# Optimization experiments

Hardware: AMD Instinct MI355X
Metric: run time of the kernel (lower is better)

The kernel has to match this reference:

```python
import jax, jax.numpy as jnp
import numpy as np
import math

B, T = 16, 512
P = 256          # num_memory_positions
E = 128          # embedding_dim
NB = 4           # num_beings
K = 4            # attention_radius
TEMP = 8.0       # attention_temperature
PHI = 1.618033988749895


def setup_inputs() -> dict:
    key = jax.random.key(0)
    ks = jax.random.split(key, 8)
    x = jax.random.normal(ks[0], (B, T, 8), jnp.float32)
    W_in = jax.random.normal(ks[1], (8, E), jnp.float32) * 0.1
    b_in = jnp.zeros((E,), jnp.float32)
    W_out = jax.random.normal(ks[2], (E, 8), jnp.float32) * 0.1
    b_out = jnp.zeros((8,), jnp.float32)
    W_p = jax.random.normal(ks[3], (E, E), jnp.float32) * (1.0 / np.sqrt(E))
    b_p = jnp.zeros((E,), jnp.float32)
    ptr_dest = jax.random.uniform(ks[4], (NB, P), jnp.float32) * P
    jump_W = jax.random.normal(ks[5], (NB, E), jnp.float32) * 0.1
    jump_b = jnp.zeros((NB,), jnp.float32)
    ctx_strength = jnp.full((NB,), 0.2, jnp.float32)
    pe = np.zeros((NB, E), np.float32)
    for i in range(NB):
        ph = i * PHI
        v = []
        for h in range(1, 9):
            v += [math.sin(h * ph), math.cos(h * ph)]
        pe[i, :16] = v  # phase_embedding padded with zeros to E (E >= 16)
    phase_bias = jnp.asarray(pe)
    seg = P / NB
    pointer_init = jax.random.uniform(ks[6], (NB, B), jnp.float32) * seg + jnp.arange(NB, dtype=jnp.float32)[:, None] * seg
    return dict(x=x, W_in=W_in, b_in=b_in, W_out=W_out, b_out=b_out,
                W_p=W_p, b_p=b_p, ptr_dest=ptr_dest, jump_W=jump_W,
                jump_b=jump_b, ctx_strength=ctx_strength,
                phase_bias=phase_bias, pointer_init=pointer_init)


def _forward(x, W_in, b_in, W_out, b_out, W_p, b_p, ptr_dest, jump_W,
             jump_b, ctx_strength, phase_bias, pointer_init):
    offsets = jnp.arange(-K, K + 1)          # [W]
    b_ix = jnp.arange(B)                     # [B]
    half = P / 2.0
    ring0 = jnp.zeros((B, P, E), x.dtype)
    hid0 = jnp.zeros((NB, B, E), x.dtype)

    def step(carry, x_t):
        ring, ptrs, hids = carry
        inp = x_t @ W_in + b_in              # [B,E]
        outs, new_ptrs, new_hids = [], [], []
        for i in range(NB):                  # beings sequential (share ring)
            ptr, hid = ptrs[i], hids[i]
            base = jnp.clip(jnp.floor(ptr).astype(jnp.int32), 0, P - 1)
            idx = (base[:, None] + offsets[None, :]) % P            # [B,W]
            delta = jnp.mod(idx.astype(x_t.dtype) - ptr[:, None] + half, P) - half
            w = jax.nn.softmax(-(delta ** 2) / TEMP, axis=1)         # [B,W]
            nbhd = ring[b_ix[:, None], idx]                          # [B,W,E]
            ctx = jnp.sum(w[..., None] * nbhd, axis=1)               # [B,E]
            comb = inp + jax.nn.sigmoid(ctx_strength[i]) * ctx + 0.1 * phase_bias[i]
            s = jnp.tanh(comb + hid)
            s = jnp.tanh(s @ W_p + b_p)      # depth-1 = 1 processing layer
            ring = ring.at[b_ix[:, None], idx].add(w[..., None] * s[:, None, :])
            cur = jnp.clip(ptr.astype(jnp.int32), 0, P - 1)
            jump_target = ptr_dest[i][cur]                           # [B]
            probs = jax.nn.sigmoid(s @ jump_W[i] + jump_b[i])        # [B]
            hard = (probs > 0.5).astype(s.dtype)
            should_jump = hard - jax.lax.stop_gradient(probs) + probs
            walk = (ptr + 1.0) % P
            new_ptrs.append(jnp.where(should_jump > 0.5, jump_target, walk))
            new_hids.append(s)
            outs.append(s @ W_out + b_out)                           # [B,8]
        out_t = jnp.mean(jnp.stack(outs), axis=0)                    # [B,8] (training-mode mean)
        return (ring, jnp.stack(new_ptrs), jnp.stack(new_hids)), out_t

    _, ys = jax.lax.scan(step, (ring0, pointer_init, hid0), jnp.swapaxes(x, 0, 1))
    return jnp.swapaxes(ys, 0, 1)            # [B,T,8]


def reference(x, W_in, b_in, W_out, b_out, W_p, b_p, ptr_dest, jump_W,
              jump_b, ctx_strength, phase_bias, pointer_init):
    return _forward(x, W_in, b_in, W_out, b_out, W_p, b_p, ptr_dest,
                    jump_W, jump_b, ctx_strength, phase_bias, pointer_init)
```

## Files before the change

### kernel.cpp

```cpp
#include <hip/hip_runtime.h>
#include <cmath>

namespace {
constexpr int B_ = 16, T_ = 512, P_ = 256, E_ = 128, NB_ = 4, K_ = 4;

__device__ __forceinline__ float rcpf(float x) { return __builtin_amdgcn_rcpf(x); }
__device__ __forceinline__ float fast_tanh(float x) {
    float a = fabsf(x);
    float t = __expf(-2.0f * a);
    float r = 1.0f - 2.0f * t * rcpf(1.0f + t);
    return copysignf(r, x);
}
__device__ __forceinline__ float redkq(float v) {
    v += __shfl_xor(v, 16);
    v += __shfl_xor(v, 32);
    return v;
}
__device__ __forceinline__ float sel4(int kq, float a, float b, float c, float d) {
    const float t0 = (kq & 1) ? b : a;
    const float t1 = (kq & 1) ? d : c;
    return (kq & 2) ? t1 : t0;
}
}

__global__ __launch_bounds__(256, 1)
void swarm_ring_kernel(const float* __restrict__ x,
                       const float* __restrict__ W_in,
                       const float* __restrict__ b_in,
                       const float* __restrict__ W_out,
                       const float* __restrict__ b_out,
                       const float* __restrict__ W_p,
                       const float* __restrict__ b_p,
                       const float* __restrict__ ptr_dest,
                       const float* __restrict__ jump_W,
                       const float* __restrict__ jump_b,
                       const float* __restrict__ ctx_strength,
                       const float* __restrict__ phase_bias,
                       const float* __restrict__ pointer_init,
                       float* __restrict__ out)
{
    __shared__ alignas(16) float  ring[P_ * E_];
    __shared__ alignas(16) float4 s4[E_];
    __shared__ alignas(16) float  sbuf[2 * E_];
    __shared__ alignas(16) float  red[16];
    __shared__ alignas(16) float  hist[16][132];
    __shared__ alignas(16) float  wout_s[8][132];

    const int tid = threadIdx.x;
    const int b   = blockIdx.x;
    const int w   = tid >> 6;
    const int l   = tid & 63;
    const int sub = l & 15;
    const int kq  = l >> 4;
    const int e0  = ((w << 4) | sub) << 1;

    for (int k4 = tid; k4 < P_ * E_ / 4; k4 += 256)
        ((float4*)ring)[k4] = make_float4(0.f, 0.f, 0.f, 0.f);
    for (int idx = tid; idx < 8 * E_; idx += 256) {
        const int m = idx >> 7, ee = idx & 127;
        wout_s[m][ee] = W_out[ee * 8 + m] * 0.25f;
    }

    float2 wp2[32];
    #pragma unroll
    for (int kk = 0; kk < 32; ++kk)
        wp2[kk] = *(const float2*)(W_p + (kq * 32 + kk) * E_ + e0);

    const float2 bin2 = *(const float2*)(b_in + e0);
    const float2 bp2  = *(const float2*)(b_p + e0);
    const float  bout_m = b_out[tid & 7];

    float2 pb2[NB_], jw2[NB_], hid2[NB_];
    float  sigc[NB_], jb_r[NB_], ptrv[NB_];
    #pragma unroll
    for (int i = 0; i < NB_; ++i) {
        const float2 pb = *(const float2*)(phase_bias + i * E_ + e0);
        pb2[i] = make_float2(0.1f * pb.x, 0.1f * pb.y);
        jw2[i] = *(const float2*)(jump_W + i * E_ + e0);
        sigc[i] = 1.0f / (1.0f + __expf(-ctx_strength[i]));
        jb_r[i] = jump_b[i];
        hid2[i] = make_float2(0.f, 0.f);
        ptrv[i] = pointer_init[i * B_ + b];
    }

    const float* xb = x + (size_t)b * T_ * 8;
    float xt[8];
    {
        float4 a0 = ((const float4*)xb)[0], a1 = ((const float4*)xb)[1];
        xt[0]=a0.x; xt[1]=a0.y; xt[2]=a0.z; xt[3]=a0.w;
        xt[4]=a1.x; xt[5]=a1.y; xt[6]=a1.z; xt[7]=a1.w;
    }

    const float Cw1 = 0.8824969f, Cw2 = 0.60653066f, Cw3 = 0.32465247f, Cw4 = 0.13533528f;
    const float Dw1 = 0.7788008f, Dw2 = 0.36787944f, Dw3 = 0.105399225f, Dw4 = 0.018315639f;

    __syncthreads();

    for (int t = 0; t < T_; ++t) {
        int   baseA[NB_];
        float fA[NB_], psinv[NB_], jt[NB_], wgt[NB_][9];
        #pragma unroll
        for (int i = 0; i < NB_; ++i) {
            const float p = ptrv[i];
            const int base = (int)p;
            baseA[i] = base;
            jt[i] = ptr_dest[i * P_ + base];
            const float f = p - (float)base;
            fA[i] = f;
            const float r  = __expf(0.25f * f);
            const float r2 = r * r, r3 = r2 * r, r4 = r2 * r2;
            const float ri = rcpf(r), ri2 = ri * ri, ri3 = ri2 * ri, ri4 = ri2 * ri2;
            const float p0 = Cw4*ri4, p1 = Cw3*ri3, p2 = Cw2*ri2, p3 = Cw1*ri, p4 = 1.0f,
                        p5 = Cw1*r,  p6 = Cw2*r2,  p7 = Cw3*r3,  p8 = Cw4*r4;
            const float sum = ((p0+p1)+(p2+p3)) + ((p4+p5)+(p6+p7)) + p8;
            const float inv = rcpf(sum);
            psinv[i] = inv;
            wgt[i][0]=p0*inv; wgt[i][1]=p1*inv; wgt[i][2]=p2*inv; wgt[i][3]=p3*inv;
            wgt[i][4]=p4*inv; wgt[i][5]=p5*inv; wgt[i][6]=p6*inv; wgt[i][7]=p7*inv;
            wgt[i][8]=p8*inv;
        }

        int ddm[NB_][NB_];
        bool overlap = false;
        #pragma unroll
        for (int j = 1; j < NB_; ++j)
            #pragma unroll
            for (int i = 0; i < j; ++i) {
                const int dd = ((baseA[j] - baseA[i] + 128) & 255) - 128;
                ddm[j][i] = dd;
                overlap = overlap || (dd >= -8 && dd <= 8);
            }

        float  ws0[NB_], ws1[NB_];
        float2 ctxp2[NB_];
        #pragma unroll
        for (int i = 0; i < NB_; ++i) {
            ws0[i] = sel4(kq, wgt[i][0], wgt[i][1], wgt[i][2], wgt[i][3]);
            ws1[i] = sel4(kq, wgt[i][4], wgt[i][5], wgt[i][6], wgt[i][7]);
            const int r0 = (baseA[i] + kq - K_) & (P_ - 1);
            const int r1 = (baseA[i] + kq + 4 - K_) & (P_ - 1);
            const float2 g0 = *(const float2*)(ring + r0 * E_ + e0);
            const float2 g1 = *(const float2*)(ring + r1 * E_ + e0);
            float cx = fmaf(ws1[i], g1.x, ws0[i] * g0.x);
            float cy = fmaf(ws1[i], g1.y, ws0[i] * g0.y);
            if (kq == 0) {
                const int r2 = (baseA[i] + 8 - K_) & (P_ - 1);
                const float2 g2 = *(const float2*)(ring + r2 * E_ + e0);
                cx = fmaf(wgt[i][8], g2.x, cx);
                cy = fmaf(wgt[i][8], g2.y, cy);
            }
            ctxp2[i] = make_float2(redkq(cx), redkq(cy));
        }

        float2 inp2 = bin2;
        #pragma unroll
        for (int k = 0; k < 8; ++k) {
            const float2 wk = *(const float2*)(W_in + k * E_ + e0);
            inp2.x = fmaf(xt[k], wk.x, inp2.x);
            inp2.y = fmaf(xt[k], wk.y, inp2.y);
        }

        float xtn[8];
        if (t + 1 < T_) {
            float4 a0 = ((const float4*)(xb + (t + 1) * 8))[0];
            float4 a1 = ((const float4*)(xb + (t + 1) * 8))[1];
            xtn[0]=a0.x; xtn[1]=a0.y; xtn[2]=a0.z; xtn[3]=a0.w;
            xtn[4]=a1.x; xtn[5]=a1.y; xtn[6]=a1.z; xtn[7]=a1.w;
        } else {
            #pragma unroll
            for (int k = 0; k < 8; ++k) xtn[k] = 0.f;
        }

        float2 sv2[NB_];

        if (!overlap) {
            float2 s1v[NB_];
            #pragma unroll
            for (int j = 0; j < NB_; ++j) {
                s1v[j].x = fast_tanh(fmaf(sigc[j], ctxp2[j].x, inp2.x + pb2[j].x + hid2[j].x));
                s1v[j].y = fast_tanh(fmaf(sigc[j], ctxp2[j].y, inp2.y + pb2[j].y + hid2[j].y));
            }
            if (kq == 0) {
                s4[e0]     = make_float4(s1v[0].x, s1v[1].x, s1v[2].x, s1v[3].x);
                s4[e0 + 1] = make_float4(s1v[0].y, s1v[1].y, s1v[2].y, s1v[3].y);
            }
            __syncthreads();

            float2 ab0 = make_float2(0.f, 0.f), ab1 = ab0, ab2 = ab0, ab3 = ab0;
            const float4* sp = s4 + kq * 32;
            #pragma unroll
            for (int kk = 0; kk < 32; ++kk) {
                const float4 sq = sp[kk];
                const float2 w2 = wp2[kk];
                ab0.x = fmaf(sq.x, w2.x, ab0.x); ab0.y = fmaf(sq.x, w2.y, ab0.y);
                ab1.x = fmaf(sq.y, w2.x, ab1.x); ab1.y = fmaf(sq.y, w2.y, ab1.y);
                ab2.x = fmaf(sq.z, w2.x, ab2.x); ab2.y = fmaf(sq.z, w2.y, ab2.y);
                ab3.x = fmaf(sq.w, w2.x, ab3.x); ab3.y = fmaf(sq.w, w2.y, ab3.y);
            }
            sv2[0] = make_float2(fast_tanh(redkq(ab0.x) + bp2.x), fast_tanh(redkq(ab0.y) + bp2.y));
            sv2[1] = make_float2(fast_tanh(redkq(ab1.x) + bp2.x), fast_tanh(redkq(ab1.y) + bp2.y));
            sv2[2] = make_float2(fast_tanh(redkq(ab2.x) + bp2.x), fast_tanh(redkq(ab2.y) + bp2.y));
            sv2[3] = make_float2(fast_tanh(redkq(ab3.x) + bp2.x), fast_tanh(redkq(ab3.y) + bp2.y));
            #pragma unroll
            for (int j = 0; j < NB_; ++j) hid2[j] = sv2[j];

            #pragma unroll
            for (int j = 0; j < NB_; ++j) {
                const float2 s = sv2[j];
                const int r0 = (baseA[j] + kq - K_) & (P_ - 1);
                float2* q0 = (float2*)(ring + r0 * E_ + e0);
                float2 v0 = *q0;
                v0.x = fmaf(ws0[j], s.x, v0.x); v0.y = fmaf(ws0[j], s.y, v0.y);
                *q0 = v0;
                const int r1 = (baseA[j] + kq + 4 - K_) & (P_ - 1);
                float2* q1 = (float2*)(ring + r1 * E_ + e0);
                float2 v1 = *q1;
                v1.x = fmaf(ws1[j], s.x, v1.x); v1.y = fmaf(ws1[j], s.y, v1.y);
                *q1 = v1;
                if (kq == 0) {
                    const int r2 = (baseA[j] + 8 - K_) & (P_ - 1);
                    float2* q2 = (float2*)(ring + r2 * E_ + e0);
                    float2 v2 = *q2;
                    v2.x = fmaf(wgt[j][8], s.x, v2.x); v2.y = fmaf(wgt[j][8], s.y, v2.y);
                    *q2 = v2;
                }
            }
        } else {
            float coefm[NB_][NB_];
            #pragma unroll
            for (int j = 1; j < NB_; ++j) {
                #pragma unroll
                for (int i = 0; i < j; ++i) {
                    const int dd = ddm[j][i];
                    float c = 0.f;
                    if (dd >= -8 && dd <= 8) {
                        const float A = (float)dd - fA[i];
                        const float s  = __expf(-0.25f * (A - fA[j]));
                        const float G  = __expf(0.125f * (fA[i] * fA[i] - A * A));
                        const float s2p = s * s, s3p = s2p * s, s4p = s2p * s2p;
                        const float si = rcpf(s), si2 = si * si, si3 = si2 * si, si4 = si2 * si2;
                        float acc = 0.f;
                        acc += (dd >= 0)              ? Dw4 * si4 : 0.f;
                        acc += (dd >= -1 && dd <= 7)  ? Dw3 * si3 : 0.f;
                        acc += (dd >= -2 && dd <= 6)  ? Dw2 * si2 : 0.f;
                        acc += (dd >= -3 && dd <= 5)  ? Dw1 * si  : 0.f;
                        acc += (dd >= -4 && dd <= 4)  ? 1.0f      : 0.f;
                        acc += (dd >= -5 && dd <= 3)  ? Dw1 * s   : 0.f;
                        acc += (dd >= -6 && dd <= 2)  ? Dw2 * s2p : 0.f;
                        acc += (dd >= -7 && dd <= 1)  ? Dw3 * s3p : 0.f;
                        acc += (dd <= 0)              ? Dw4 * s4p : 0.f;
                        c = psinv[i] * psinv[j] * G * acc;
                    }
                    coefm[j][i] = c;
                }
            }

            #pragma unroll
            for (int j = 0; j < NB_; ++j) {
                float2 ctx = ctxp2[j];
                #pragma unroll
                for (int i = 0; i < j; ++i) {
                    ctx.x = fmaf(coefm[j][i], sv2[i].x, ctx.x);
                    ctx.y = fmaf(coefm[j][i], sv2[i].y, ctx.y);
                }
                float2 s1;
                s1.x = fast_tanh(fmaf(sigc[j], ctx.x, inp2.x + pb2[j].x + hid2[j].x));
                s1.y = fast_tanh(fmaf(sigc[j], ctx.y, inp2.y + pb2[j].y + hid2[j].y));
                if (kq == 0) *(float2*)(sbuf + (j & 1) * E_ + e0) = s1;
                __syncthreads();

                const float4* sp = (const float4*)(sbuf + (j & 1) * E_) + kq * 8;
                float ax = 0.f, ay = 0.f;
                #pragma unroll
                for (int kk = 0; kk < 8; ++kk) {
                    const float4 sq = sp[kk];
                    const float2 wa = wp2[4 * kk + 0], wb = wp2[4 * kk + 1];
                    const float2 wc = wp2[4 * kk + 2], wd = wp2[4 * kk + 3];
                    ax = fmaf(sq.x, wa.x, ax); ay = fmaf(sq.x, wa.y, ay);
                    ax = fmaf(sq.y, wb.x, ax); ay = fmaf(sq.y, wb.y, ay);
                    ax = fmaf(sq.z, wc.x, ax); ay = fmaf(sq.z, wc.y, ay);
                    ax = fmaf(sq.w, wd.x, ax); ay = fmaf(sq.w, wd.y, ay);
                }
                float2 s2;
                s2.x = fast_tanh(redkq(ax) + bp2.x);
                s2.y = fast_tanh(redkq(ay) + bp2.y);
                sv2[j] = s2; hid2[j] = s2;

                const int r0 = (baseA[j] + kq - K_) & (P_ - 1);
                float2* q0 = (float2*)(ring + r0 * E_ + e0);
                float2 v0 = *q0;
                v0.x = fmaf(ws0[j], s2.x, v0.x); v0.y = fmaf(ws0[j], s2.y, v0.y);
                *q0 = v0;
                const int r1 = (baseA[j] + kq + 4 - K_) & (P_ - 1);
                float2* q1 = (float2*)(ring + r1 * E_ + e0);
                float2 v1 = *q1;
                v1.x = fmaf(ws1[j], s2.x, v1.x); v1.y = fmaf(ws1[j], s2.y, v1.y);
                *q1 = v1;
                if (kq == 0) {
                    const int r2 = (baseA[j] + 8 - K_) & (P_ - 1);
                    float2* q2 = (float2*)(ring + r2 * E_ + e0);
                    float2 v2 = *q2;
                    v2.x = fmaf(wgt[j][8], s2.x, v2.x); v2.y = fmaf(wgt[j][8], s2.y, v2.y);
                    *q2 = v2;
                }
            }
        }

        {
            float vj0 = fmaf(sv2[0].y, jw2[0].y, sv2[0].x * jw2[0].x);
            float vj1 = fmaf(sv2[1].y, jw2[1].y, sv2[1].x * jw2[1].x);
            float vj2 = fmaf(sv2[2].y, jw2[2].y, sv2[2].x * jw2[2].x);
            float vj3 = fmaf(sv2[3].y, jw2[3].y, sv2[3].x * jw2[3].x);
            #pragma unroll
            for (int off = 1; off < 16; off <<= 1) {
                vj0 += __shfl_xor(vj0, off);
                vj1 += __shfl_xor(vj1, off);
                vj2 += __shfl_xor(vj2, off);
                vj3 += __shfl_xor(vj3, off);
            }
            if (l == 0)
                ((float4*)red)[w] = make_float4(vj0, vj1, vj2, vj3);
        }

        {
            float2 ssum2;
            ssum2.x = (sv2[0].x + sv2[1].x) + (sv2[2].x + sv2[3].x);
            ssum2.y = (sv2[0].y + sv2[1].y) + (sv2[2].y + sv2[3].y);
            if (kq == 0) *(float2*)(&hist[t & 15][e0]) = ssum2;
        }

        __syncthreads();

        {
            const float4 r0 = ((const float4*)red)[0];
            const float4 r1 = ((const float4*)red)[1];
            const float4 r2 = ((const float4*)red)[2];
            const float4 r3 = ((const float4*)red)[3];
            const float zz[4] = {
                ((r0.x + r1.x) + (r2.x + r3.x)) + jb_r[0],
                ((r0.y + r1.y) + (r2.y + r3.y)) + jb_r[1],
                ((r0.z + r1.z) + (r2.z + r3.z)) + jb_r[2],
                ((r0.w + r1.w) + (r2.w + r3.w)) + jb_r[3]};
            #pragma unroll
            for (int i = 0; i < NB_; ++i) {
                float np;
                if (zz[i] > 0.0f) np = jt[i];
                else { np = ptrv[i] + 1.0f; if (np >= 256.0f) np -= 256.0f; }
                ptrv[i] = np;
            }
        }

        if ((t & 7) == 7 && tid < 64) {
            const int tt = tid >> 3;
            const int m  = tid & 7;
            const float* hrow = hist[(t - 7 + tt) & 15];
            const float* wrow = wout_s[m];
            float acc = 0.f;
            #pragma unroll
            for (int q = 0; q < 32; ++q) {
                const float4 h4 = ((const float4*)hrow)[q];
                const float4 w4 = ((const float4*)wrow)[q];
                acc += ((h4.x * w4.x + h4.y * w4.y) + (h4.z * w4.z + h4.w * w4.w));
            }
            out[((size_t)b * T_ + (t - 7 + tt)) * 8 + m] = acc + bout_m;
        }

        #pragma unroll
        for (int k = 0; k < 8; ++k) xt[k] = xtn[k];
    }
}

extern "C" void kernel_launch(void* const* d_in, const int* in_sizes, int n_in,
                              void* d_out, int out_size, void* d_ws, size_t ws_size,
                              hipStream_t stream) {
    (void)in_sizes; (void)n_in; (void)out_size; (void)d_ws; (void)ws_size;
    swarm_ring_kernel<<<dim3(B_), dim3(256), 0, stream>>>(
        (const float*)d_in[0],  (const float*)d_in[1],  (const float*)d_in[2],
        (const float*)d_in[3],  (const float*)d_in[4],  (const float*)d_in[5],
        (const float*)d_in[6],  (const float*)d_in[7],  (const float*)d_in[8],
        (const float*)d_in[9],  (const float*)d_in[10], (const float*)d_in[11],
        (const float*)d_in[12], (float*)d_out);
}
```

Before: 2.056 ms.

## Double threads per block so each thread handles one embedding column

Raises the block from 256 to 512 threads so each lane owns a single embedding element instead of a pair. This halves the per-thread serial work in the latency-bound recurrent step. The shared-memory state buffer gets padding (stride 33) and the jump-logit reduction grows from 4 to 8 wave partials. The cost is twice as many waves meeting at each barrier and more shuffle and reduction traffic per step.

```diff
diff --git a/kernel.cpp b/kernel.cpp
--- a/kernel.cpp
+++ b/kernel.cpp
@@ -3,6 +3,7 @@
 
 namespace {
 constexpr int B_ = 16, T_ = 512, P_ = 256, E_ = 128, NB_ = 4, K_ = 4;
+constexpr int THREADS_ = 512;
 
 __device__ __forceinline__ float rcpf(float x) { return __builtin_amdgcn_rcpf(x); }
 __device__ __forceinline__ float fast_tanh(float x) {
@@ -23,7 +24,7 @@
 }
 }
 
-__global__ __launch_bounds__(256, 1)
+__global__ __launch_bounds__(512, 1)
 void swarm_ring_kernel(const float* __restrict__ x,
                        const float* __restrict__ W_in,
                        const float* __restrict__ b_in,
@@ -40,9 +41,9 @@
                        float* __restrict__ out)
 {
     __shared__ alignas(16) float  ring[P_ * E_];
-    __shared__ alignas(16) float4 s4[E_];
-    __shared__ alignas(16) float  sbuf[2 * E_];
-    __shared__ alignas(16) float  red[16];
+    __shared__ alignas(16) float4 s4[132];
+    __shared__ alignas(16) float  sbuf[2][4][36];
+    __shared__ alignas(16) float  red[32];
     __shared__ alignas(16) float  hist[16][132];
     __shared__ alignas(16) float  wout_s[8][132];
 
@@ -52,34 +53,38 @@
     const int l   = tid & 63;
     const int sub = l & 15;
     const int kq  = l >> 4;
-    const int e0  = ((w << 4) | sub) << 1;
-
-    for (int k4 = tid; k4 < P_ * E_ / 4; k4 += 256)
+    const int e   = (w << 4) | sub;
+
+    for (int k4 = tid; k4 < P_ * E_ / 4; k4 += THREADS_)
         ((float4*)ring)[k4] = make_float4(0.f, 0.f, 0.f, 0.f);
-    for (int idx = tid; idx < 8 * E_; idx += 256) {
+    for (int idx = tid; idx < 8 * E_; idx += THREADS_) {
         const int m = idx >> 7, ee = idx & 127;
         wout_s[m][ee] = W_out[ee * 8 + m] * 0.25f;
     }
 
-    float2 wp2[32];
+    float wp[32];
     #pragma unroll
     for (int kk = 0; kk < 32; ++kk)
-        wp2[kk] = *(const float2*)(W_p + (kq * 32 + kk) * E_ + e0);
-
-    const float2 bin2 = *(const float2*)(b_in + e0);
-    const float2 bp2  = *(const float2*)(b_p + e0);
-    const float  bout_m = b_out[tid & 7];
-
-    float2 pb2[NB_], jw2[NB_], hid2[NB_];
-    float  sigc[NB_], jb_r[NB_], ptrv[NB_];
+        wp[kk] = W_p[(kq * 32 + kk) * E_ + e];
+
+    float wi[8];
+    #pragma unroll
+    for (int k = 0; k < 8; ++k)
+        wi[k] = W_in[k * E_ + e];
+
+    const float bin_r  = b_in[e];
+    const float bp_r   = b_p[e];
+    const float bout_m = b_out[tid & 7];
+
+    float pb_r[NB_], jw_r[NB_], hid_r[NB_];
+    float sigc[NB_], jb_r[NB_], ptrv[NB_];
     #pragma unroll
     for (int i = 0; i < NB_; ++i) {
-        const float2 pb = *(const float2*)(phase_bias + i * E_ + e0);
-        pb2[i] = make_float2(0.1f * pb.x, 0.1f * pb.y);
-        jw2[i] = *(const float2*)(jump_W + i * E_ + e0);
+        pb_r[i] = 0.1f * phase_bias[i * E_ + e];
+        jw_r[i] = jump_W[i * E_ + e];
         sigc[i] = 1.0f / (1.0f + __expf(-ctx_strength[i]));
         jb_r[i] = jump_b[i];
-        hid2[i] = make_float2(0.f, 0.f);
+        hid_r[i] = 0.f;
         ptrv[i] = pointer_init[i * B_ + b];
     }
 
@@ -131,34 +136,28 @@
                 overlap = overlap || (dd >= -8 && dd <= 8);
             }
 
-        float  ws0[NB_], ws1[NB_];
-        float2 ctxp2[NB_];
+        float ws0[NB_], ws1[NB_];
+        float ctxp[NB_];
         #pragma unroll
         for (int i = 0; i < NB_; ++i) {
             ws0[i] = sel4(kq, wgt[i][0], wgt[i][1], wgt[i][2], wgt[i][3]);
             ws1[i] = sel4(kq, wgt[i][4], wgt[i][5], wgt[i][6], wgt[i][7]);
             const int r0 = (baseA[i] + kq - K_) & (P_ - 1);
             const int r1 = (baseA[i] + kq + 4 - K_) & (P_ - 1);
-            const float2 g0 = *(const float2*)(ring + r0 * E_ + e0);
-            const float2 g1 = *(const float2*)(ring + r1 * E_ + e0);
-            float cx = fmaf(ws1[i], g1.x, ws0[i] * g0.x);
-            float cy = fmaf(ws1[i], g1.y, ws0[i] * g0.y);
+            const float g0 = ring[r0 * E_ + e];
+            const float g1 = ring[r1 * E_ + e];
+            float c = fmaf(ws1[i], g1, ws0[i] * g0);
             if (kq == 0) {
                 const int r2 = (baseA[i] + 8 - K_) & (P_ - 1);
-                const float2 g2 = *(const float2*)(ring + r2 * E_ + e0);
-                cx = fmaf(wgt[i][8], g2.x, cx);
-                cy = fmaf(wgt[i][8], g2.y, cy);
-            }
-            ctxp2[i] = make_float2(redkq(cx), redkq(cy));
-        }
-
-        float2 inp2 = bin2;
-        #pragma unroll
-        for (int k = 0; k < 8; ++k) {
-            const float2 wk = *(const float2*)(W_in + k * E_ + e0);
-            inp2.x = fmaf(xt[k], wk.x, inp2.x);
-            inp2.y = fmaf(xt[k], wk.y, inp2.y);
-        }
+                c = fmaf(wgt[i][8], ring[r2 * E_ + e], c);
+            }
+            ctxp[i] = redkq(c);
+        }
+
+        float inp = bin_r;
+        #pragma unroll
+        for (int k = 0; k < 8; ++k)
+            inp = fmaf(xt[k], wi[k], inp);
 
         float xtn[8];
         if (t + 1 < T_) {
@@ -171,58 +170,45 @@
             for (int k = 0; k < 8; ++k) xtn[k] = 0.f;
         }
 
-        float2 sv2[NB_];
+        float sv[NB_];
 
         if (!overlap) {
-            float2 s1v[NB_];
-            #pragma unroll
-            for (int j = 0; j < NB_; ++j) {
-                s1v[j].x = fast_tanh(fmaf(sigc[j], ctxp2[j].x, inp2.x + pb2[j].x + hid2[j].x));
-                s1v[j].y = fast_tanh(fmaf(sigc[j], ctxp2[j].y, inp2.y + pb2[j].y + hid2[j].y));
-            }
-            if (kq == 0) {
-                s4[e0]     = make_float4(s1v[0].x, s1v[1].x, s1v[2].x, s1v[3].x);
-                s4[e0 + 1] = make_float4(s1v[0].y, s1v[1].y, s1v[2].y, s1v[3].y);
-            }
+            float s1v[NB_];
+            #pragma unroll
+            for (int j = 0; j < NB_; ++j)
+                s1v[j] = fast_tanh(fmaf(sigc[j], ctxp[j], inp + pb_r[j] + hid_r[j]));
+            if (kq == 0)
+                s4[e + (e >> 5)] = make_float4(s1v[0], s1v[1], s1v[2], s1v[3]);
             __syncthreads();
 
-            float2 ab0 = make_float2(0.f, 0.f), ab1 = ab0, ab2 = ab0, ab3 = ab0;
-            const float4* sp = s4 + kq * 32;
+            float ab0 = 0.f, ab1 = 0.f, ab2 = 0.f, ab3 = 0.f;
+            const float4* sp = s4 + kq * 33;
             #pragma unroll
             for (int kk = 0; kk < 32; ++kk) {
                 const float4 sq = sp[kk];
-                const float2 w2 = wp2[kk];
-                ab0.x = fmaf(sq.x, w2.x, ab0.x); ab0.y = fmaf(sq.x, w2.y, ab0.y);
-                ab1.x = fmaf(sq.y, w2.x, ab1.x); ab1.y = fmaf(sq.y, w2.y, ab1.y);
-                ab2.x = fmaf(sq.z, w2.x, ab2.x); ab2.y = fmaf(sq.z, w2.y, ab2.y);
-                ab3.x = fmaf(sq.w, w2.x, ab3.x); ab3.y = fmaf(sq.w, w2.y, ab3.y);
-            }
-            sv2[0] = make_float2(fast_tanh(redkq(ab0.x) + bp2.x), fast_tanh(redkq(ab0.y) + bp2.y));
-            sv2[1] = make_float2(fast_tanh(redkq(ab1.x) + bp2.x), fast_tanh(redkq(ab1.y) + bp2.y));
-            sv2[2] = make_float2(fast_tanh(redkq(ab2.x) + bp2.x), fast_tanh(redkq(ab2.y) + bp2.y));
-            sv2[3] = make_float2(fast_tanh(redkq(ab3.x) + bp2.x), fast_tanh(redkq(ab3.y) + bp2.y));
-            #pragma unroll
-            for (int j = 0; j < NB_; ++j) hid2[j] = sv2[j];
+                const float wk = wp[kk];
+                ab0 = fmaf(sq.x, wk, ab0);
+                ab1 = fmaf(sq.y, wk, ab1);
+                ab2 = fmaf(sq.z, wk, ab2);
+                ab3 = fmaf(sq.w, wk, ab3);
+            }
+            sv[0] = fast_tanh(redkq(ab0) + bp_r);
+            sv[1] = fast_tanh(redkq(ab1) + bp_r);
+            sv[2] = fast_tanh(redkq(ab2) + bp_r);
+            sv[3] = fast_tanh(redkq(ab3) + bp_r);
+            #pragma unroll
+            for (int j = 0; j < NB_; ++j) hid_r[j] = sv[j];
 
             #pragma unroll
             for (int j = 0; j < NB_; ++j) {
-                const float2 s = sv2[j];
+                const float s = sv[j];
                 const int r0 = (baseA[j] + kq - K_) & (P_ - 1);
-                float2* q0 = (float2*)(ring + r0 * E_ + e0);
-                float2 v0 = *q0;
-                v0.x = fmaf(ws0[j], s.x, v0.x); v0.y = fmaf(ws0[j], s.y, v0.y);
-                *q0 = v0;
+                ring[r0 * E_ + e] = fmaf(ws0[j], s, ring[r0 * E_ + e]);
                 const int r1 = (baseA[j] + kq + 4 - K_) & (P_ - 1);
-                float2* q1 = (float2*)(ring + r1 * E_ + e0);
-                float2 v1 = *q1;
-                v1.x = fmaf(ws1[j], s.x, v1.x); v1.y = fmaf(ws1[j], s.y, v1.y);
-                *q1 = v1;
+                ring[r1 * E_ + e] = fmaf(ws1[j], s, ring[r1 * E_ + e]);
                 if (kq == 0) {
                     const int r2 = (baseA[j] + 8 - K_) & (P_ - 1);
-                    float2* q2 = (float2*)(ring + r2 * E_ + e0);
-                    float2 v2 = *q2;
-                    v2.x = fmaf(wgt[j][8], s.x, v2.x); v2.y = fmaf(wgt[j][8], s.y, v2.y);
-                    *q2 = v2;
+                    ring[r2 * E_ + e] = fmaf(wgt[j][8], s, ring[r2 * E_ + e]);
                 }
             }
         } else {
@@ -257,60 +243,43 @@
 
             #pragma unroll
             for (int j = 0; j < NB_; ++j) {
-                float2 ctx = ctxp2[j];
+                float ctx = ctxp[j];
                 #pragma unroll
-                for (int i = 0; i < j; ++i) {
-                    ctx.x = fmaf(coefm[j][i], sv2[i].x, ctx.x);
-                    ctx.y = fmaf(coefm[j][i], sv2[i].y, ctx.y);
-                }
-                float2 s1;
-                s1.x = fast_tanh(fmaf(sigc[j], ctx.x, inp2.x + pb2[j].x + hid2[j].x));
-                s1.y = fast_tanh(fmaf(sigc[j], ctx.y, inp2.y + pb2[j].y + hid2[j].y));
-                if (kq == 0) *(float2*)(sbuf + (j & 1) * E_ + e0) = s1;
+                for (int i = 0; i < j; ++i)
+                    ctx = fmaf(coefm[j][i], sv[i], ctx);
+                const float s1 = fast_tanh(fmaf(sigc[j], ctx, inp + pb_r[j] + hid_r[j]));
+                if (kq == 0) sbuf[j & 1][e >> 5][e & 31] = s1;
                 __syncthreads();
 
-                const float4* sp = (const float4*)(sbuf + (j & 1) * E_) + kq * 8;
-                float ax = 0.f, ay = 0.f;
+                const float4* sp4 = (const float4*)(sbuf[j & 1][kq]);
+                float ax = 0.f;
                 #pragma unroll
                 for (int kk = 0; kk < 8; ++kk) {
-                    const float4 sq = sp[kk];
-                    const float2 wa = wp2[4 * kk + 0], wb = wp2[4 * kk + 1];
-                    const float2 wc = wp2[4 * kk + 2], wd = wp2[4 * kk + 3];
-                    ax = fmaf(sq.x, wa.x, ax); ay = fmaf(sq.x, wa.y, ay);
-                    ax = fmaf(sq.y, wb.x, ax); ay = fmaf(sq.y, wb.y, ay);
-                    ax = fmaf(sq.z, wc.x, ax); ay = fmaf(sq.z, wc.y, ay);
-                    ax = fmaf(sq.w, wd.x, ax); ay = fmaf(sq.w, wd.y, ay);
+                    const float4 sq = sp4[kk];
+                    ax = fmaf(sq.x, wp[4 * kk + 0], ax);
+                    ax = fmaf(sq.y, wp[4 * kk + 1], ax);
+                    ax = fmaf(sq.z, wp[4 * kk + 2], ax);
+                    ax = fmaf(sq.w, wp[4 * kk + 3], ax);
                 }
-                float2 s2;
-                s2.x = fast_tanh(redkq(ax) + bp2.x);
-                s2.y = fast_tanh(redkq(ay) + bp2.y);
-                sv2[j] = s2; hid2[j] = s2;
+                const float s2 = fast_tanh(redkq(ax) + bp_r);
+                sv[j] = s2; hid_r[j] = s2;
 
                 const int r0 = (baseA[j] + kq - K_) & (P_ - 1);
-                float2* q0 = (float2*)(ring + r0 * E_ + e0);
-                float2 v0 = *q0;
-                v0.x = fmaf(ws0[j], s2.x, v0.x); v0.y = fmaf(ws0[j], s2.y, v0.y);
-                *q0 = v0;
+                ring[r0 * E_ + e] = fmaf(ws0[j], s2, ring[r0 * E_ + e]);
                 const int r1 = (baseA[j] + kq + 4 - K_) & (P_ - 1);
-                float2* q1 = (float2*)(ring + r1 * E_ + e0);
-                float2 v1 = *q1;
-                v1.x = fmaf(ws1[j], s2.x, v1.x); v1.y = fmaf(ws1[j], s2.y, v1.y);
-                *q1 = v1;
+                ring[r1 * E_ + e] = fmaf(ws1[j], s2, ring[r1 * E_ + e]);
                 if (kq == 0) {
                     const int r2 = (baseA[j] + 8 - K_) & (P_ - 1);
-                    float2* q2 = (float2*)(ring + r2 * E_ + e0);
-                    float2 v2 = *q2;
-                    v2.x = fmaf(wgt[j][8], s2.x, v2.x); v2.y = fmaf(wgt[j][8], s2.y, v2.y);
-                    *q2 = v2;
+                    ring[r2 * E_ + e] = fmaf(wgt[j][8], s2, ring[r2 * E_ + e]);
                 }
             }
         }
 
         {
-            float vj0 = fmaf(sv2[0].y, jw2[0].y, sv2[0].x * jw2[0].x);
-            float vj1 = fmaf(sv2[1].y, jw2[1].y, sv2[1].x * jw2[1].x);
-            float vj2 = fmaf(sv2[2].y, jw2[2].y, sv2[2].x * jw2[2].x);
-            float vj3 = fmaf(sv2[3].y, jw2[3].y, sv2[3].x * jw2[3].x);
+            float vj0 = sv[0] * jw_r[0];
+            float vj1 = sv[1] * jw_r[1];
+            float vj2 = sv[2] * jw_r[2];
+            float vj3 = sv[3] * jw_r[3];
             #pragma unroll
             for (int off = 1; off < 16; off <<= 1) {
                 vj0 += __shfl_xor(vj0, off);
@@ -323,10 +292,8 @@
         }
 
         {
-            float2 ssum2;
-            ssum2.x = (sv2[0].x + sv2[1].x) + (sv2[2].x + sv2[3].x);
-            ssum2.y = (sv2[0].y + sv2[1].y) + (sv2[2].y + sv2[3].y);
-            if (kq == 0) *(float2*)(&hist[t & 15][e0]) = ssum2;
+            const float ssum = (sv[0] + sv[1]) + (sv[2] + sv[3]);
+            if (kq == 0) hist[t & 15][e] = ssum;
         }
 
         __syncthreads();
@@ -336,11 +303,15 @@
             const float4 r1 = ((const float4*)red)[1];
             const float4 r2 = ((const float4*)red)[2];
             const float4 r3 = ((const float4*)red)[3];
+            const float4 r4 = ((const float4*)red)[4];
+            const float4 r5 = ((const float4*)red)[5];
+            const float4 r6 = ((const float4*)red)[6];
+            const float4 r7 = ((const float4*)red)[7];
             const float zz[4] = {
-                ((r0.x + r1.x) + (r2.x + r3.x)) + jb_r[0],
-                ((r0.y + r1.y) + (r2.y + r3.y)) + jb_r[1],
-                ((r0.z + r1.z) + (r2.z + r3.z)) + jb_r[2],
-                ((r0.w + r1.w) + (r2.w + r3.w)) + jb_r[3]};
+                (((r0.x + r1.x) + (r2.x + r3.x)) + ((r4.x + r5.x) + (r6.x + r7.x))) + jb_r[0],
+                (((r0.y + r1.y) + (r2.y + r3.y)) + ((r4.y + r5.y) + (r6.y + r7.y))) + jb_r[1],
+                (((r0.z + r1.z) + (r2.z + r3.z)) + ((r4.z + r5.z) + (r6.z + r7.z))) + jb_r[2],
+                (((r0.w + r1.w) + (r2.w + r3.w)) + ((r4.w + r5.w) + (r6.w + r7.w))) + jb_r[3]};
             #pragma unroll
             for (int i = 0; i < NB_; ++i) {
                 float np;
@@ -374,7 +345,7 @@
                               void* d_out, int out_size, void* d_ws, size_t ws_size,
                               hipStream_t stream) {
     (void)in_sizes; (void)n_in; (void)out_size; (void)d_ws; (void)ws_size;
-    swarm_ring_kernel<<<dim3(B_), dim3(256), 0, stream>>>(
+    swarm_ring_kernel<<<dim3(B_), dim3(THREADS_), 0, stream>>>(
         (const float*)d_in[0],  (const float*)d_in[1],  (const float*)d_in[2],
         (const float*)d_in[3],  (const float*)d_in[4],  (const float*)d_in[5],
         (const float*)d_in[6],  (const float*)d_in[7],  (const float*)d_in[8],
```

New measurement: 1.994 ms. -3.0%, faster.

## Double block to 512 threads, split K reduction 8-way with DPP/permlane reductions

Applied to the files above, without the earlier changes.

Raises the block size from 256 to 512 threads so each wave covers 8 embedding pairs with 8 K-quarters instead of 4, halving per-thread W_p registers and ring accesses per step. Reductions across the K-split now use DPP row shifts and permlane16/32 swaps instead of shuffles. The ring row stride is padded to 132, and the s4/sbuf layouts are padded to reduce LDS bank conflicts. W_in is also hoisted into registers. The cost is more barrier participants per step and new cross-lane instruction sequences whose correctness depends on the DPP control encodings.

```diff
diff --git a/kernel.cpp b/kernel.cpp
--- a/kernel.cpp
+++ b/kernel.cpp
@@ -3,6 +3,8 @@
 
 namespace {
 constexpr int B_ = 16, T_ = 512, P_ = 256, E_ = 128, NB_ = 4, K_ = 4;
+constexpr int THREADS_ = 512;
+constexpr int RS_ = 132;
 
 __device__ __forceinline__ float rcpf(float x) { return __builtin_amdgcn_rcpf(x); }
 __device__ __forceinline__ float fast_tanh(float x) {
@@ -11,19 +13,60 @@
     float r = 1.0f - 2.0f * t * rcpf(1.0f + t);
     return copysignf(r, x);
 }
-__device__ __forceinline__ float redkq(float v) {
-    v += __shfl_xor(v, 16);
-    v += __shfl_xor(v, 32);
+
+template<int CTRL>
+__device__ __forceinline__ float dpp_addf(float v) {
+    const int s = __builtin_amdgcn_update_dpp(0, __float_as_int(v), CTRL, 0xF, 0xF, true);
+    return v + __int_as_float(s);
+}
+template<int Q>
+__device__ __forceinline__ float dpp_bcast4(float v) {
+    const int s = __builtin_amdgcn_update_dpp(0, __float_as_int(v), Q * 0x55, 0xF, 0xF, true);
+    return __int_as_float(s);
+}
+__device__ __forceinline__ float pl16_sum(float v) {
+#if __has_builtin(__builtin_amdgcn_permlane16_swap)
+    const unsigned u = __float_as_uint(v);
+    const auto r = __builtin_amdgcn_permlane16_swap(u, u, false, false);
+    return __uint_as_float(r[0]) + __uint_as_float(r[1]);
+#else
+    return v + __shfl_xor(v, 16);
+#endif
+}
+__device__ __forceinline__ float pl32_sum(float v) {
+#if __has_builtin(__builtin_amdgcn_permlane32_swap)
+    const unsigned u = __float_as_uint(v);
+    const auto r = __builtin_amdgcn_permlane32_swap(u, u, false, false);
+    return __uint_as_float(r[0]) + __uint_as_float(r[1]);
+#else
+    return v + __shfl_xor(v, 32);
+#endif
+}
+__device__ __forceinline__ float redkq8(float v) {
+    v = dpp_addf<0x128>(v);
+    v = pl16_sum(v);
+    v = pl32_sum(v);
     return v;
 }
-__device__ __forceinline__ float sel4(int kq, float a, float b, float c, float d) {
-    const float t0 = (kq & 1) ? b : a;
-    const float t1 = (kq & 1) ? d : c;
-    return (kq & 2) ? t1 : t0;
-}
-}
-
-__global__ __launch_bounds__(256, 1)
+__device__ __forceinline__ float redpair(float v) {
+    v = dpp_addf<0xB1>(v);
+    v = dpp_addf<0x4E>(v);
+    v = dpp_addf<0x141>(v);
+    return v;
+}
+__device__ __forceinline__ float sel8f(int kq, float w0, float w1, float w2, float w3,
+                                       float w4, float w5, float w6, float w7) {
+    const float a = (kq & 1) ? w1 : w0;
+    const float b = (kq & 1) ? w3 : w2;
+    const float c = (kq & 1) ? w5 : w4;
+    const float d = (kq & 1) ? w7 : w6;
+    const float e = (kq & 2) ? b : a;
+    const float f = (kq & 2) ? d : c;
+    return (kq & 4) ? f : e;
+}
+}
+
+__global__ __launch_bounds__(512, 1)
 void swarm_ring_kernel(const float* __restrict__ x,
                        const float* __restrict__ W_in,
                        const float* __restrict__ b_in,
@@ -39,10 +82,10 @@
                        const float* __restrict__ pointer_init,
                        float* __restrict__ out)
 {
-    __shared__ alignas(16) float  ring[P_ * E_];
-    __shared__ alignas(16) float4 s4[E_];
-    __shared__ alignas(16) float  sbuf[2 * E_];
-    __shared__ alignas(16) float  red[16];
+    __shared__ alignas(16) float  ring[P_ * RS_];
+    __shared__ alignas(16) float4 s4[136];
+    __shared__ alignas(16) float  sbuf[2][160];
+    __shared__ alignas(16) float  red[32];
     __shared__ alignas(16) float  hist[16][132];
     __shared__ alignas(16) float  wout_s[8][132];
 
@@ -50,21 +93,26 @@
     const int b   = blockIdx.x;
     const int w   = tid >> 6;
     const int l   = tid & 63;
-    const int sub = l & 15;
-    const int kq  = l >> 4;
-    const int e0  = ((w << 4) | sub) << 1;
-
-    for (int k4 = tid; k4 < P_ * E_ / 4; k4 += 256)
+    const int s_  = l & 7;
+    const int kq  = l >> 3;
+    const int e0  = ((w << 3) | s_) << 1;
+
+    for (int k4 = tid; k4 < P_ * RS_ / 4; k4 += THREADS_)
         ((float4*)ring)[k4] = make_float4(0.f, 0.f, 0.f, 0.f);
-    for (int idx = tid; idx < 8 * E_; idx += 256) {
+    for (int idx = tid; idx < 8 * E_; idx += THREADS_) {
         const int m = idx >> 7, ee = idx & 127;
         wout_s[m][ee] = W_out[ee * 8 + m] * 0.25f;
     }
 
-    float2 wp2[32];
+    float2 wp2[16];
     #pragma unroll
-    for (int kk = 0; kk < 32; ++kk)
-        wp2[kk] = *(const float2*)(W_p + (kq * 32 + kk) * E_ + e0);
+    for (int kk = 0; kk < 16; ++kk)
+        wp2[kk] = *(const float2*)(W_p + (kq * 16 + kk) * E_ + e0);
+
+    float2 wi2[8];
+    #pragma unroll
+    for (int k = 0; k < 8; ++k)
+        wi2[k] = *(const float2*)(W_in + k * E_ + e0);
 
     const float2 bin2 = *(const float2*)(b_in + e0);
     const float2 bp2  = *(const float2*)(b_p + e0);
@@ -131,33 +179,31 @@
                 overlap = overlap || (dd >= -8 && dd <= 8);
             }
 
-        float  ws0[NB_], ws1[NB_];
+        float  ws[NB_], w8[NB_];
         float2 ctxp2[NB_];
         #pragma unroll
         for (int i = 0; i < NB_; ++i) {
-            ws0[i] = sel4(kq, wgt[i][0], wgt[i][1], wgt[i][2], wgt[i][3]);
-            ws1[i] = sel4(kq, wgt[i][4], wgt[i][5], wgt[i][6], wgt[i][7]);
+            ws[i] = sel8f(kq, wgt[i][0], wgt[i][1], wgt[i][2], wgt[i][3],
+                              wgt[i][4], wgt[i][5], wgt[i][6], wgt[i][7]);
+            w8[i] = wgt[i][8];
             const int r0 = (baseA[i] + kq - K_) & (P_ - 1);
-            const int r1 = (baseA[i] + kq + 4 - K_) & (P_ - 1);
-            const float2 g0 = *(const float2*)(ring + r0 * E_ + e0);
-            const float2 g1 = *(const float2*)(ring + r1 * E_ + e0);
-            float cx = fmaf(ws1[i], g1.x, ws0[i] * g0.x);
-            float cy = fmaf(ws1[i], g1.y, ws0[i] * g0.y);
+            const float2 g0 = *(const float2*)(ring + r0 * RS_ + e0);
+            float cx = ws[i] * g0.x;
+            float cy = ws[i] * g0.y;
             if (kq == 0) {
-                const int r2 = (baseA[i] + 8 - K_) & (P_ - 1);
-                const float2 g2 = *(const float2*)(ring + r2 * E_ + e0);
-                cx = fmaf(wgt[i][8], g2.x, cx);
-                cy = fmaf(wgt[i][8], g2.y, cy);
-            }
-            ctxp2[i] = make_float2(redkq(cx), redkq(cy));
+                const int r2 = (baseA[i] + K_) & (P_ - 1);
+                const float2 g2 = *(const float2*)(ring + r2 * RS_ + e0);
+                cx = fmaf(w8[i], g2.x, cx);
+                cy = fmaf(w8[i], g2.y, cy);
+            }
+            ctxp2[i] = make_float2(redkq8(cx), redkq8(cy));
         }
 
         float2 inp2 = bin2;
         #pragma unroll
         for (int k = 0; k < 8; ++k) {
-            const float2 wk = *(const float2*)(W_in + k * E_ + e0);
-            inp2.x = fmaf(xt[k], wk.x, inp2.x);
-            inp2.y = fmaf(xt[k], wk.y, inp2.y);
+            inp2.x = fmaf(xt[k], wi2[k].x, inp2.x);
+            inp2.y = fmaf(xt[k], wi2[k].y, inp2.y);
         }
 
         float xtn[8];
@@ -181,15 +227,16 @@
                 s1v[j].y = fast_tanh(fmaf(sigc[j], ctxp2[j].y, inp2.y + pb2[j].y + hid2[j].y));
             }
             if (kq == 0) {
-                s4[e0]     = make_float4(s1v[0].x, s1v[1].x, s1v[2].x, s1v[3].x);
-                s4[e0 + 1] = make_float4(s1v[0].y, s1v[1].y, s1v[2].y, s1v[3].y);
+                const int si = 17 * w + (s_ << 1);
+                s4[si]     = make_float4(s1v[0].x, s1v[1].x, s1v[2].x, s1v[3].x);
+                s4[si + 1] = make_float4(s1v[0].y, s1v[1].y, s1v[2].y, s1v[3].y);
             }
             __syncthreads();
 
             float2 ab0 = make_float2(0.f, 0.f), ab1 = ab0, ab2 = ab0, ab3 = ab0;
-            const float4* sp = s4 + kq * 32;
-            #pragma unroll
-            for (int kk = 0; kk < 32; ++kk) {
+            const float4* sp = s4 + kq * 17;
+            #pragma unroll
+            for (int kk = 0; kk < 16; ++kk) {
                 const float4 sq = sp[kk];
                 const float2 w2 = wp2[kk];
                 ab0.x = fmaf(sq.x, w2.x, ab0.x); ab0.y = fmaf(sq.x, w2.y, ab0.y);
@@ -197,10 +244,10 @@
                 ab2.x = fmaf(sq.z, w2.x, ab2.x); ab2.y = fmaf(sq.z, w2.y, ab2.y);
                 ab3.x = fmaf(sq.w, w2.x, ab3.x); ab3.y = fmaf(sq.w, w2.y, ab3.y);
             }
-            sv2[0] = make_float2(fast_tanh(redkq(ab0.x) + bp2.x), fast_tanh(redkq(ab0.y) + bp2.y));
-            sv2[1] = make_float2(fast_tanh(redkq(ab1.x) + bp2.x), fast_tanh(redkq(ab1.y) + bp2.y));
-            sv2[2] = make_float2(fast_tanh(redkq(ab2.x) + bp2.x), fast_tanh(redkq(ab2.y) + bp2.y));
-            sv2[3] = make_float2(fast_tanh(redkq(ab3.x) + bp2.x), fast_tanh(redkq(ab3.y) + bp2.y));
+            sv2[0] = make_float2(fast_tanh(redkq8(ab0.x) + bp2.x), fast_tanh(redkq8(ab0.y) + bp2.y));
+            sv2[1] = make_float2(fast_tanh(redkq8(ab1.x) + bp2.x), fast_tanh(redkq8(ab1.y) + bp2.y));
+            sv2[2] = make_float2(fast_tanh(redkq8(ab2.x) + bp2.x), fast_tanh(redkq8(ab2.y) + bp2.y));
+            sv2[3] = make_float2(fast_tanh(redkq8(ab3.x) + bp2.x), fast_tanh(redkq8(ab3.y) + bp2.y));
             #pragma unroll
             for (int j = 0; j < NB_; ++j) hid2[j] = sv2[j];
 
@@ -208,20 +255,15 @@
             for (int j = 0; j < NB_; ++j) {
                 const float2 s = sv2[j];
                 const int r0 = (baseA[j] + kq - K_) & (P_ - 1);
-                float2* q0 = (float2*)(ring + r0 * E_ + e0);
+                float2* q0 = (float2*)(ring + r0 * RS_ + e0);
                 float2 v0 = *q0;
-                v0.x = fmaf(ws0[j], s.x, v0.x); v0.y = fmaf(ws0[j], s.y, v0.y);
+                v0.x = fmaf(ws[j], s.x, v0.x); v0.y = fmaf(ws[j], s.y, v0.y);
                 *q0 = v0;
-                const int r1 = (baseA[j] + kq + 4 - K_) & (P_ - 1);
-                float2* q1 = (float2*)(ring + r1 * E_ + e0);
-                float2 v1 = *q1;
-                v1.x = fmaf(ws1[j], s.x, v1.x); v1.y = fmaf(ws1[j], s.y, v1.y);
-                *q1 = v1;
                 if (kq == 0) {
-                    const int r2 = (baseA[j] + 8 - K_) & (P_ - 1);
-                    float2* q2 = (float2*)(ring + r2 * E_ + e0);
+                    const int r2 = (baseA[j] + K_) & (P_ - 1);
+                    float2* q2 = (float2*)(ring + r2 * RS_ + e0);
                     float2 v2 = *q2;
-                    v2.x = fmaf(wgt[j][8], s.x, v2.x); v2.y = fmaf(wgt[j][8], s.y, v2.y);
+                    v2.x = fmaf(w8[j], s.x, v2.x); v2.y = fmaf(w8[j], s.y, v2.y);
                     *q2 = v2;
                 }
             }
@@ -266,41 +308,39 @@
                 float2 s1;
                 s1.x = fast_tanh(fmaf(sigc[j], ctx.x, inp2.x + pb2[j].x + hid2[j].x));
                 s1.y = fast_tanh(fmaf(sigc[j], ctx.y, inp2.y + pb2[j].y + hid2[j].y));
-                if (kq == 0) *(float2*)(sbuf + (j & 1) * E_ + e0) = s1;
+                if (kq == 0) {
+                    const int pf = 20 * w + (s_ << 1);
+                    *(float2*)(&sbuf[j & 1][pf]) = s1;
+                }
                 __syncthreads();
 
-                const float4* sp = (const float4*)(sbuf + (j & 1) * E_) + kq * 8;
+                const float4* sp4 = (const float4*)(&sbuf[j & 1][0]);
                 float ax = 0.f, ay = 0.f;
                 #pragma unroll
-                for (int kk = 0; kk < 8; ++kk) {
-                    const float4 sq = sp[kk];
-                    const float2 wa = wp2[4 * kk + 0], wb = wp2[4 * kk + 1];
-                    const float2 wc = wp2[4 * kk + 2], wd = wp2[4 * kk + 3];
+                for (int m = 0; m < 4; ++m) {
+                    const float4 sq = sp4[5 * kq + m];
+                    const float2 wa = wp2[4*m+0], wb = wp2[4*m+1];
+                    const float2 wc = wp2[4*m+2], wd = wp2[4*m+3];
                     ax = fmaf(sq.x, wa.x, ax); ay = fmaf(sq.x, wa.y, ay);
                     ax = fmaf(sq.y, wb.x, ax); ay = fmaf(sq.y, wb.y, ay);
                     ax = fmaf(sq.z, wc.x, ax); ay = fmaf(sq.z, wc.y, ay);
                     ax = fmaf(sq.w, wd.x, ax); ay = fmaf(sq.w, wd.y, ay);
                 }
                 float2 s2;
-                s2.x = fast_tanh(redkq(ax) + bp2.x);
-                s2.y = fast_tanh(redkq(ay) + bp2.y);
+                s2.x = fast_tanh(redkq8(ax) + bp2.x);
+                s2.y = fast_tanh(redkq8(ay) + bp2.y);
                 sv2[j] = s2; hid2[j] = s2;
 
                 const int r0 = (baseA[j] + kq - K_) & (P_ - 1);
-                float2* q0 = (float2*)(ring + r0 * E_ + e0);
+                float2* q0 = (float2*)(ring + r0 * RS_ + e0);
                 float2 v0 = *q0;
-                v0.x = fmaf(ws0[j], s2.x, v0.x); v0.y = fmaf(ws0[j], s2.y, v0.y);
+                v0.x = fmaf(ws[j], s2.x, v0.x); v0.y = fmaf(ws[j], s2.y, v0.y);
                 *q0 = v0;
-                const int r1 = (baseA[j] + kq + 4 - K_) & (P_ - 1);
-                float2* q1 = (float2*)(ring + r1 * E_ + e0);
-                float2 v1 = *q1;
-                v1.x = fmaf(ws1[j], s2.x, v1.x); v1.y = fmaf(ws1[j], s2.y, v1.y);
-                *q1 = v1;
                 if (kq == 0) {
-                    const int r2 = (baseA[j] + 8 - K_) & (P_ - 1);
-                    float2* q2 = (float2*)(ring + r2 * E_ + e0);
+                    const int r2 = (baseA[j] + K_) & (P_ - 1);
+                    float2* q2 = (float2*)(ring + r2 * RS_ + e0);
                     float2 v2 = *q2;
-                    v2.x = fmaf(wgt[j][8], s2.x, v2.x); v2.y = fmaf(wgt[j][8], s2.y, v2.y);
+                    v2.x = fmaf(w8[j], s2.x, v2.x); v2.y = fmaf(w8[j], s2.y, v2.y);
                     *q2 = v2;
                 }
             }
@@ -311,13 +351,7 @@
             float vj1 = fmaf(sv2[1].y, jw2[1].y, sv2[1].x * jw2[1].x);
             float vj2 = fmaf(sv2[2].y, jw2[2].y, sv2[2].x * jw2[2].x);
             float vj3 = fmaf(sv2[3].y, jw2[3].y, sv2[3].x * jw2[3].x);
-            #pragma unroll
-            for (int off = 1; off < 16; off <<= 1) {
-                vj0 += __shfl_xor(vj0, off);
-                vj1 += __shfl_xor(vj1, off);
-                vj2 += __shfl_xor(vj2, off);
-                vj3 += __shfl_xor(vj3, off);
-            }
+            vj0 = redpair(vj0); vj1 = redpair(vj1); vj2 = redpair(vj2); vj3 = redpair(vj3);
             if (l == 0)
                 ((float4*)red)[w] = make_float4(vj0, vj1, vj2, vj3);
         }
@@ -332,15 +366,15 @@
         __syncthreads();
 
         {
-            const float4 r0 = ((const float4*)red)[0];
-            const float4 r1 = ((const float4*)red)[1];
-            const float4 r2 = ((const float4*)red)[2];
-            const float4 r3 = ((const float4*)red)[3];
-            const float zz[4] = {
-                ((r0.x + r1.x) + (r2.x + r3.x)) + jb_r[0],
-                ((r0.y + r1.y) + (r2.y + r3.y)) + jb_r[1],
-                ((r0.z + r1.z) + (r2.z + r3.z)) + jb_r[2],
-                ((r0.w + r1.w) + (r2.w + r3.w)) + jb_r[3]};
+            float rv = red[l & 31];
+            rv = dpp_addf<0x124>(rv);
+            rv = dpp_addf<0x128>(rv);
+            rv = pl16_sum(rv);
+            const float zz0 = dpp_bcast4<0>(rv) + jb_r[0];
+            const float zz1 = dpp_bcast4<1>(rv) + jb_r[1];
+            const float zz2 = dpp_bcast4<2>(rv) + jb_r[2];
+            const float zz3 = dpp_bcast4<3>(rv) + jb_r[3];
+            const float zz[4] = { zz0, zz1, zz2, zz3 };
             #pragma unroll
             for (int i = 0; i < NB_; ++i) {
                 float np;
@@ -374,7 +408,7 @@
                               void* d_out, int out_size, void* d_ws, size_t ws_size,
                               hipStream_t stream) {
     (void)in_sizes; (void)n_in; (void)out_size; (void)d_ws; (void)ws_size;
-    swarm_ring_kernel<<<dim3(B_), dim3(256), 0, stream>>>(
+    swarm_ring_kernel<<<dim3(B_), dim3(THREADS_), 0, stream>>>(
         (const float*)d_in[0],  (const float*)d_in[1],  (const float*)d_in[2],
         (const float*)d_in[3],  (const float*)d_in[4],  (const float*)d_in[5],
         (const float*)d_in[6],  (const float*)d_in[7],  (const float*)d_in[8],
```

After: 2.032 ms. Within noise of the previous version (-1.2%).
